# Kernel optimization log

Measured on AMD Instinct MI355X. Metric: run time of the kernel, lower is better.

The kernel has to match this reference:

```python
import jax, jax.numpy as jnp
import numpy as np

N_NODES = 40000


def _gcn_conv(x, edge_index, W, b):
    """PyG GCNConv: add self-loops, symmetric degree normalization,
    linear transform, gather-scale-scatter aggregation, bias."""
    n = x.shape[0]
    loops = jnp.arange(n, dtype=edge_index.dtype)
    src = jnp.concatenate([edge_index[0], loops])  # [E+N]
    dst = jnp.concatenate([edge_index[1], loops])  # [E+N]
    ones = jnp.ones(src.shape[0], dtype=x.dtype)
    deg = jax.ops.segment_sum(ones, dst, num_segments=n)  # in-degree incl. self-loop
    dinv = jnp.where(deg > 0, jax.lax.rsqrt(deg), 0.0)
    norm = dinv[src] * dinv[dst]  # [E+N]
    h = x @ W  # [n, out]
    msg = h[src] * norm[:, None]  # [E+N, out] gather + scale
    out = jax.ops.segment_sum(msg, dst, num_segments=n)  # scatter-add
    return out + b


def setup_inputs() -> dict:
    key = jax.random.key(0)
    k = jax.random.split(key, 6)
    n, din, dh, dout = N_NODES, 128, 128, 64
    x = jax.random.normal(k[0], (n, din), dtype=jnp.float32)
    edge_index = jax.random.randint(k[1], (2, 640000), 0, n, dtype=jnp.int64)
    W1 = jax.random.normal(k[2], (din, dh), dtype=jnp.float32) / np.sqrt(din)
    b1 = jnp.zeros((dh,), dtype=jnp.float32)
    W2 = jax.random.normal(k[3], (dh, dout), dtype=jnp.float32) / np.sqrt(dh)
    b2 = jnp.zeros((dout,), dtype=jnp.float32)
    return {"x": x, "edge_index": edge_index, "W1": W1, "b1": b1, "W2": W2, "b2": b2}


def reference(x, edge_index, W1, b1, W2, b2):
    h = jax.nn.relu(_gcn_conv(x, edge_index, W1, b1))
    return _gcn_conv(h, edge_index, W2, b2)
```

## Files before the change

### kernel.cpp

```cpp
#include <hip/hip_runtime.h>
#include <hip/hip_fp16.h>


#define N_NODES 40000
#define DIN 128
#define DH 128
#define DOUT 64
#define NEDGES 640000
#define CAP 64
#define NBUCKET 2560
#define I4_PER_CHUNK 500
#define NODES_PER_XCD 5000
#define NCVT 1250
#define NWT 8

typedef _Float16 f16x8 __attribute__((ext_vector_type(8)));
typedef float f32x4 __attribute__((ext_vector_type(4)));

__global__ __launch_bounds__(256) void k_bkt_cvt(
    const float* __restrict__ x, _Float16* __restrict__ xh,
    const int4* __restrict__ src4, const int4* __restrict__ dst4,
    int* __restrict__ deg, unsigned short* __restrict__ ssrc,
    const float* __restrict__ W1, const float* __restrict__ W2,
    _Float16* __restrict__ WT1, _Float16* __restrict__ WT2)
{
    if (blockIdx.x < NBUCKET) {
        const int xg = blockIdx.x & 7;
        const int c  = blockIdx.x >> 3;
        const int lo = xg * NODES_PER_XCD, hi = lo + NODES_PER_XCD;
        const int e0 = c * I4_PER_CHUNK, e1 = e0 + I4_PER_CHUNK;
        for (int e = e0 + threadIdx.x; e < e1; e += 256) {
            int4 d = dst4[e];
            int4 s = src4[e];
            if (d.x >= lo && d.x < hi) {
                int p = atomicAdd(&deg[d.x], 1);
                if (p < CAP) ssrc[d.x * CAP + p] = (unsigned short)s.x;
            }
            if (d.y >= lo && d.y < hi) {
                int p = atomicAdd(&deg[d.y], 1);
                if (p < CAP) ssrc[d.y * CAP + p] = (unsigned short)s.y;
            }
            if (d.z >= lo && d.z < hi) {
                int p = atomicAdd(&deg[d.z], 1);
                if (p < CAP) ssrc[d.z * CAP + p] = (unsigned short)s.z;
            }
            if (d.w >= lo && d.w < hi) {
                int p = atomicAdd(&deg[d.w], 1);
                if (p < CAP) ssrc[d.w * CAP + p] = (unsigned short)s.w;
            }
        }
    } else if (blockIdx.x < NBUCKET + NCVT) {
        const size_t base = ((size_t)(blockIdx.x - NBUCKET) * 256 + threadIdx.x) * 16;
        float4 a0 = *(const float4*)(x + base);
        float4 a1 = *(const float4*)(x + base + 4);
        float4 a2 = *(const float4*)(x + base + 8);
        float4 a3 = *(const float4*)(x + base + 12);
        f16x8 o0 = { (_Float16)a0.x, (_Float16)a0.y, (_Float16)a0.z, (_Float16)a0.w,
                     (_Float16)a1.x, (_Float16)a1.y, (_Float16)a1.z, (_Float16)a1.w };
        f16x8 o1 = { (_Float16)a2.x, (_Float16)a2.y, (_Float16)a2.z, (_Float16)a2.w,
                     (_Float16)a3.x, (_Float16)a3.y, (_Float16)a3.z, (_Float16)a3.w };
        *(f16x8*)(xh + base)     = o0;
        *(f16x8*)(xh + base + 8) = o1;
    } else {
        const int b = blockIdx.x - NBUCKET - NCVT;
        for (int i = b * 256 + threadIdx.x; i < DIN * DH; i += NWT * 256) {
            int k = i >> 7, nn = i & 127;
            WT1[nn * DIN + k] = (_Float16)W1[i];
        }
        for (int i = b * 256 + threadIdx.x; i < DH * DOUT; i += NWT * 256) {
            int k = i >> 6, nn = i & 63;
            WT2[nn * DH + k] = (_Float16)W2[i];
        }
    }
}

__global__ __launch_bounds__(256) void k_scale(
    _Float16* __restrict__ xh, const int* __restrict__ deg)
{
    int idx = blockIdx.x * 256 + threadIdx.x;
    int row = idx >> 4;
    float dn = rsqrtf((float)(deg[row] + 1));
    f16x8 v = *(f16x8*)(xh + (size_t)idx * 8);
    f16x8 o;
#pragma unroll
    for (int j = 0; j < 8; ++j) o[j] = (_Float16)((float)v[j] * dn);
    *(f16x8*)(xh + (size_t)idx * 8) = o;
}

__global__ __launch_bounds__(256) void k_agg_g12(
    const int* __restrict__ deg, const unsigned short* __restrict__ ssrc,
    const _Float16* __restrict__ xh, const float* __restrict__ b1,
    const _Float16* __restrict__ WT1, const _Float16* __restrict__ WT2,
    _Float16* __restrict__ h2)
{
    __shared__ _Float16 ys[16][136];
    __shared__ _Float16 zs[16][136];
    const int w = threadIdx.x >> 6;
    const int lane = threadIdx.x & 63;
    const int g  = lane >> 4;
    const int gl = lane & 15;
    const int node0 = blockIdx.x * 16;
    const int node = node0 + w * 4 + g;

    const int dg = deg[node];
    const int cnt = min(dg, CAP);
    const float dn = rsqrtf((float)(dg + 1));

    float ac[8];
    {
        f16x8 self = *(const f16x8*)(xh + (size_t)node * DIN + gl * 8);
#pragma unroll
        for (int j = 0; j < 8; ++j) ac[j] = (float)self[j];
    }
    int mc = cnt;
    mc = max(mc, __shfl_xor(mc, 16));
    mc = max(mc, __shfl_xor(mc, 32));

    const unsigned short* bin = ssrc + (size_t)node * CAP;
    for (int e = 0; e < mc; e += 8) {
        uint4 pk = *(const uint4*)(bin + e);
        int s0 = (int)(pk.x & 0xFFFF), s1 = (int)(pk.x >> 16);
        int s2 = (int)(pk.y & 0xFFFF), s3 = (int)(pk.y >> 16);
        int s4 = (int)(pk.z & 0xFFFF), s5 = (int)(pk.z >> 16);
        int s6 = (int)(pk.w & 0xFFFF), s7 = (int)(pk.w >> 16);
        float m0 = (e + 0 < cnt) ? 1.f : 0.f;  s0 = (e + 0 < cnt) ? s0 : node;
        float m1 = (e + 1 < cnt) ? 1.f : 0.f;  s1 = (e + 1 < cnt) ? s1 : node;
        float m2 = (e + 2 < cnt) ? 1.f : 0.f;  s2 = (e + 2 < cnt) ? s2 : node;
        float m3 = (e + 3 < cnt) ? 1.f : 0.f;  s3 = (e + 3 < cnt) ? s3 : node;
        float m4 = (e + 4 < cnt) ? 1.f : 0.f;  s4 = (e + 4 < cnt) ? s4 : node;
        float m5 = (e + 5 < cnt) ? 1.f : 0.f;  s5 = (e + 5 < cnt) ? s5 : node;
        float m6 = (e + 6 < cnt) ? 1.f : 0.f;  s6 = (e + 6 < cnt) ? s6 : node;
        float m7 = (e + 7 < cnt) ? 1.f : 0.f;  s7 = (e + 7 < cnt) ? s7 : node;
        f16x8 r0 = *(const f16x8*)(xh + (size_t)s0 * DIN + gl * 8);
        f16x8 r1 = *(const f16x8*)(xh + (size_t)s1 * DIN + gl * 8);
        f16x8 r2 = *(const f16x8*)(xh + (size_t)s2 * DIN + gl * 8);
        f16x8 r3 = *(const f16x8*)(xh + (size_t)s3 * DIN + gl * 8);
        f16x8 r4 = *(const f16x8*)(xh + (size_t)s4 * DIN + gl * 8);
        f16x8 r5 = *(const f16x8*)(xh + (size_t)s5 * DIN + gl * 8);
        f16x8 r6 = *(const f16x8*)(xh + (size_t)s6 * DIN + gl * 8);
        f16x8 r7 = *(const f16x8*)(xh + (size_t)s7 * DIN + gl * 8);
#pragma unroll
        for (int j = 0; j < 8; ++j) {
            ac[j] += (m0 * (float)r0[j] + m1 * (float)r1[j])
                   + (m2 * (float)r2[j] + m3 * (float)r3[j]);
            ac[j] += (m4 * (float)r4[j] + m5 * (float)r5[j])
                   + (m6 * (float)r6[j] + m7 * (float)r7[j]);
        }
    }
    {
        f16x8 o;
#pragma unroll
        for (int j = 0; j < 8; ++j) o[j] = (_Float16)(dn * ac[j]);
        *(f16x8*)&ys[w * 4 + g][gl * 8] = o;
    }
    __syncthreads();

    const int m = lane & 15, quad = lane >> 4;
#pragma unroll
    for (int t = 0; t < 2; ++t) {
        const int nt = w * 2 + t;
        f32x4 acc1 = (f32x4){0.f, 0.f, 0.f, 0.f};
#pragma unroll
        for (int ks = 0; ks < 4; ++ks) {
            f16x8 a = *(const f16x8*)&ys[m][ks * 32 + quad * 8];
            f16x8 b = *(const f16x8*)(WT1 + (size_t)(nt * 16 + m) * DIN + ks * 32 + quad * 8);
            acc1 = __builtin_amdgcn_mfma_f32_16x16x32_f16(a, b, acc1, 0, 0, 0);
        }
        float bias = b1[nt * 16 + m];
#pragma unroll
        for (int r = 0; r < 4; ++r) {
            float v = acc1[r] + bias;
            zs[quad * 4 + r][nt * 16 + m] = (_Float16)(v > 0.f ? v : 0.f);
        }
    }
    __syncthreads();

    {
        f32x4 acc2 = (f32x4){0.f, 0.f, 0.f, 0.f};
#pragma unroll
        for (int ks = 0; ks < 4; ++ks) {
            f16x8 a = *(const f16x8*)&zs[m][ks * 32 + quad * 8];
            f16x8 b = *(const f16x8*)(WT2 + (size_t)(w * 16 + m) * DH + ks * 32 + quad * 8);
            acc2 = __builtin_amdgcn_mfma_f32_16x16x32_f16(a, b, acc2, 0, 0, 0);
        }
#pragma unroll
        for (int r = 0; r < 4; ++r) {
            int nrow = node0 + quad * 4 + r;
            float dnr = rsqrtf((float)(deg[nrow] + 1));
            h2[(size_t)nrow * DOUT + w * 16 + m] = (_Float16)(acc2[r] * dnr);
        }
    }
}

__global__ __launch_bounds__(256) void k_agg2(
    const int* __restrict__ deg, const unsigned short* __restrict__ ssrc,
    const _Float16* __restrict__ h2, const float* __restrict__ b2,
    float* __restrict__ out)
{
    const int w = threadIdx.x >> 6;
    const int lane = threadIdx.x & 63;
    const int g  = lane >> 3;
    const int gl = lane & 7;
    const int node = blockIdx.x * 32 + w * 8 + g;

    const int dg = deg[node];
    const int cnt = min(dg, CAP);
    const float dn = rsqrtf((float)(dg + 1));

    float ac[8];
    {
        f16x8 self = *(const f16x8*)(h2 + (size_t)node * DOUT + gl * 8);
#pragma unroll
        for (int j = 0; j < 8; ++j) ac[j] = (float)self[j];
    }
    int mc = cnt;
    mc = max(mc, __shfl_xor(mc, 8));
    mc = max(mc, __shfl_xor(mc, 16));
    mc = max(mc, __shfl_xor(mc, 32));

    const unsigned short* bin = ssrc + (size_t)node * CAP;
    for (int e = 0; e < mc; e += 8) {
        uint4 pk = *(const uint4*)(bin + e);
        int s0 = (int)(pk.x & 0xFFFF), s1 = (int)(pk.x >> 16);
        int s2 = (int)(pk.y & 0xFFFF), s3 = (int)(pk.y >> 16);
        int s4 = (int)(pk.z & 0xFFFF), s5 = (int)(pk.z >> 16);
        int s6 = (int)(pk.w & 0xFFFF), s7 = (int)(pk.w >> 16);
        float m0 = (e + 0 < cnt) ? 1.f : 0.f;  s0 = (e + 0 < cnt) ? s0 : node;
        float m1 = (e + 1 < cnt) ? 1.f : 0.f;  s1 = (e + 1 < cnt) ? s1 : node;
        float m2 = (e + 2 < cnt) ? 1.f : 0.f;  s2 = (e + 2 < cnt) ? s2 : node;
        float m3 = (e + 3 < cnt) ? 1.f : 0.f;  s3 = (e + 3 < cnt) ? s3 : node;
        float m4 = (e + 4 < cnt) ? 1.f : 0.f;  s4 = (e + 4 < cnt) ? s4 : node;
        float m5 = (e + 5 < cnt) ? 1.f : 0.f;  s5 = (e + 5 < cnt) ? s5 : node;
        float m6 = (e + 6 < cnt) ? 1.f : 0.f;  s6 = (e + 6 < cnt) ? s6 : node;
        float m7 = (e + 7 < cnt) ? 1.f : 0.f;  s7 = (e + 7 < cnt) ? s7 : node;
        f16x8 r0 = *(const f16x8*)(h2 + (size_t)s0 * DOUT + gl * 8);
        f16x8 r1 = *(const f16x8*)(h2 + (size_t)s1 * DOUT + gl * 8);
        f16x8 r2 = *(const f16x8*)(h2 + (size_t)s2 * DOUT + gl * 8);
        f16x8 r3 = *(const f16x8*)(h2 + (size_t)s3 * DOUT + gl * 8);
        f16x8 r4 = *(const f16x8*)(h2 + (size_t)s4 * DOUT + gl * 8);
        f16x8 r5 = *(const f16x8*)(h2 + (size_t)s5 * DOUT + gl * 8);
        f16x8 r6 = *(const f16x8*)(h2 + (size_t)s6 * DOUT + gl * 8);
        f16x8 r7 = *(const f16x8*)(h2 + (size_t)s7 * DOUT + gl * 8);
#pragma unroll
        for (int j = 0; j < 8; ++j) {
            ac[j] += (m0 * (float)r0[j] + m1 * (float)r1[j])
                   + (m2 * (float)r2[j] + m3 * (float)r3[j]);
            ac[j] += (m4 * (float)r4[j] + m5 * (float)r5[j])
                   + (m6 * (float)r6[j] + m7 * (float)r7[j]);
        }
    }
    float4 ba = *(const float4*)(b2 + gl * 8);
    float4 bb = *(const float4*)(b2 + gl * 8 + 4);
    float4 o0 = { dn * ac[0] + ba.x, dn * ac[1] + ba.y,
                  dn * ac[2] + ba.z, dn * ac[3] + ba.w };
    float4 o1 = { dn * ac[4] + bb.x, dn * ac[5] + bb.y,
                  dn * ac[6] + bb.z, dn * ac[7] + bb.w };
    float* orow = out + (size_t)node * DOUT + gl * 8;
    *(float4*)orow = o0;
    *(float4*)(orow + 4) = o1;
}

extern "C" void kernel_launch(void* const* d_in, const int* in_sizes, int n_in,
                              void* d_out, int out_size, void* d_ws, size_t ws_size,
                              hipStream_t stream) {
    const float* x  = (const float*)d_in[0];
    const int*   ei = (const int*)d_in[1];
    const float* W1 = (const float*)d_in[2];
    const float* b1 = (const float*)d_in[3];
    const float* W2 = (const float*)d_in[4];
    const float* b2 = (const float*)d_in[5];
    float* out = (float*)d_out;

    const int n = N_NODES, E = NEDGES;
    const int* src = ei;
    const int* dst = ei + E;

    char* ws = (char*)d_ws;
    int*            deg  = (int*)(ws + 0);
    _Float16*       WT1  = (_Float16*)(ws + 163840);
    _Float16*       WT2  = (_Float16*)(ws + 196608);
    unsigned short* ssrc = (unsigned short*)(ws + 212992);
    _Float16*       xh   = (_Float16*)(ws + 5332992);
    _Float16*       h2   = (_Float16*)(ws + 15572992);

    hipMemsetAsync(deg, 0, N_NODES * sizeof(int), stream);
    k_bkt_cvt <<<NBUCKET + NCVT + NWT, 256, 0, stream>>>(x, xh, (const int4*)src,
                                                         (const int4*)dst, deg, ssrc,
                                                         W1, W2, WT1, WT2);
    k_scale   <<<(N_NODES * DIN / 8) / 256, 256, 0, stream>>>(xh, deg);
    k_agg_g12 <<<n / 16, 256, 0, stream>>>(deg, ssrc, xh, b1, WT1, WT2, h2);
    k_agg2    <<<n / 32, 256, 0, stream>>>(deg, ssrc, h2, b2, out);
}
```

Measured before the change: 158.8 us.

## Replicate per-node edge counters and bins four ways to reduce atomic contention

Bucketing now spreads each node's incoming edges over four replica sub-bins of 32 slots, selected by chunk index. Each replica has its own atomic counter, so fewer concurrent atomics hit the same address. Degree becomes the sum of four counters, read as one int4. Both aggregation kernels now loop over the four sub-bins, each padded to a multiple of 8. That adds masked gather iterations and shuffle reductions, enlarges the bin and counter memory and the memset, and caps each replica at 32 edges.

```diff
diff --git a/kernel.cpp b/kernel.cpp
--- a/kernel.cpp
+++ b/kernel.cpp
@@ -7,7 +7,7 @@
 #define DH 128
 #define DOUT 64
 #define NEDGES 640000
-#define CAP 64
+#define CAPR 32
 #define NBUCKET 2560
 #define I4_PER_CHUNK 500
 #define NODES_PER_XCD 5000
@@ -20,33 +20,34 @@
 __global__ __launch_bounds__(256) void k_bkt_cvt(
     const float* __restrict__ x, _Float16* __restrict__ xh,
     const int4* __restrict__ src4, const int4* __restrict__ dst4,
-    int* __restrict__ deg, unsigned short* __restrict__ ssrc,
+    int* __restrict__ dcnt, unsigned short* __restrict__ rbin,
     const float* __restrict__ W1, const float* __restrict__ W2,
     _Float16* __restrict__ WT1, _Float16* __restrict__ WT2)
 {
     if (blockIdx.x < NBUCKET) {
         const int xg = blockIdx.x & 7;
         const int c  = blockIdx.x >> 3;
+        const int rep = c & 3;
         const int lo = xg * NODES_PER_XCD, hi = lo + NODES_PER_XCD;
         const int e0 = c * I4_PER_CHUNK, e1 = e0 + I4_PER_CHUNK;
         for (int e = e0 + threadIdx.x; e < e1; e += 256) {
             int4 d = dst4[e];
             int4 s = src4[e];
             if (d.x >= lo && d.x < hi) {
-                int p = atomicAdd(&deg[d.x], 1);
-                if (p < CAP) ssrc[d.x * CAP + p] = (unsigned short)s.x;
+                int p = atomicAdd(&dcnt[d.x * 4 + rep], 1);
+                if (p < CAPR) rbin[(size_t)d.x * 128 + rep * CAPR + p] = (unsigned short)s.x;
             }
             if (d.y >= lo && d.y < hi) {
-                int p = atomicAdd(&deg[d.y], 1);
-                if (p < CAP) ssrc[d.y * CAP + p] = (unsigned short)s.y;
+                int p = atomicAdd(&dcnt[d.y * 4 + rep], 1);
+                if (p < CAPR) rbin[(size_t)d.y * 128 + rep * CAPR + p] = (unsigned short)s.y;
             }
             if (d.z >= lo && d.z < hi) {
-                int p = atomicAdd(&deg[d.z], 1);
-                if (p < CAP) ssrc[d.z * CAP + p] = (unsigned short)s.z;
+                int p = atomicAdd(&dcnt[d.z * 4 + rep], 1);
+                if (p < CAPR) rbin[(size_t)d.z * 128 + rep * CAPR + p] = (unsigned short)s.z;
             }
             if (d.w >= lo && d.w < hi) {
-                int p = atomicAdd(&deg[d.w], 1);
-                if (p < CAP) ssrc[d.w * CAP + p] = (unsigned short)s.w;
+                int p = atomicAdd(&dcnt[d.w * 4 + rep], 1);
+                if (p < CAPR) rbin[(size_t)d.w * 128 + rep * CAPR + p] = (unsigned short)s.w;
             }
         }
     } else if (blockIdx.x < NBUCKET + NCVT) {
@@ -75,11 +76,12 @@
 }
 
 __global__ __launch_bounds__(256) void k_scale(
-    _Float16* __restrict__ xh, const int* __restrict__ deg)
+    _Float16* __restrict__ xh, const int* __restrict__ dcnt)
 {
     int idx = blockIdx.x * 256 + threadIdx.x;
     int row = idx >> 4;
-    float dn = rsqrtf((float)(deg[row] + 1));
+    int4 dc = *(const int4*)(dcnt + row * 4);
+    float dn = rsqrtf((float)(dc.x + dc.y + dc.z + dc.w + 1));
     f16x8 v = *(f16x8*)(xh + (size_t)idx * 8);
     f16x8 o;
 #pragma unroll
@@ -88,7 +90,7 @@
 }
 
 __global__ __launch_bounds__(256) void k_agg_g12(
-    const int* __restrict__ deg, const unsigned short* __restrict__ ssrc,
+    const int* __restrict__ dcnt, const unsigned short* __restrict__ rbin,
     const _Float16* __restrict__ xh, const float* __restrict__ b1,
     const _Float16* __restrict__ WT1, const _Float16* __restrict__ WT2,
     _Float16* __restrict__ h2)
@@ -102,8 +104,8 @@
     const int node0 = blockIdx.x * 16;
     const int node = node0 + w * 4 + g;
 
-    const int dg = deg[node];
-    const int cnt = min(dg, CAP);
+    const int4 dc = *(const int4*)(dcnt + node * 4);
+    const int dg = dc.x + dc.y + dc.z + dc.w;
     const float dn = rsqrtf((float)(dg + 1));
 
     float ac[8];
@@ -112,39 +114,44 @@
 #pragma unroll
         for (int j = 0; j < 8; ++j) ac[j] = (float)self[j];
     }
-    int mc = cnt;
-    mc = max(mc, __shfl_xor(mc, 16));
-    mc = max(mc, __shfl_xor(mc, 32));
-
-    const unsigned short* bin = ssrc + (size_t)node * CAP;
-    for (int e = 0; e < mc; e += 8) {
-        uint4 pk = *(const uint4*)(bin + e);
-        int s0 = (int)(pk.x & 0xFFFF), s1 = (int)(pk.x >> 16);
-        int s2 = (int)(pk.y & 0xFFFF), s3 = (int)(pk.y >> 16);
-        int s4 = (int)(pk.z & 0xFFFF), s5 = (int)(pk.z >> 16);
-        int s6 = (int)(pk.w & 0xFFFF), s7 = (int)(pk.w >> 16);
-        float m0 = (e + 0 < cnt) ? 1.f : 0.f;  s0 = (e + 0 < cnt) ? s0 : node;
-        float m1 = (e + 1 < cnt) ? 1.f : 0.f;  s1 = (e + 1 < cnt) ? s1 : node;
-        float m2 = (e + 2 < cnt) ? 1.f : 0.f;  s2 = (e + 2 < cnt) ? s2 : node;
-        float m3 = (e + 3 < cnt) ? 1.f : 0.f;  s3 = (e + 3 < cnt) ? s3 : node;
-        float m4 = (e + 4 < cnt) ? 1.f : 0.f;  s4 = (e + 4 < cnt) ? s4 : node;
-        float m5 = (e + 5 < cnt) ? 1.f : 0.f;  s5 = (e + 5 < cnt) ? s5 : node;
-        float m6 = (e + 6 < cnt) ? 1.f : 0.f;  s6 = (e + 6 < cnt) ? s6 : node;
-        float m7 = (e + 7 < cnt) ? 1.f : 0.f;  s7 = (e + 7 < cnt) ? s7 : node;
-        f16x8 r0 = *(const f16x8*)(xh + (size_t)s0 * DIN + gl * 8);
-        f16x8 r1 = *(const f16x8*)(xh + (size_t)s1 * DIN + gl * 8);
-        f16x8 r2 = *(const f16x8*)(xh + (size_t)s2 * DIN + gl * 8);
-        f16x8 r3 = *(const f16x8*)(xh + (size_t)s3 * DIN + gl * 8);
-        f16x8 r4 = *(const f16x8*)(xh + (size_t)s4 * DIN + gl * 8);
-        f16x8 r5 = *(const f16x8*)(xh + (size_t)s5 * DIN + gl * 8);
-        f16x8 r6 = *(const f16x8*)(xh + (size_t)s6 * DIN + gl * 8);
-        f16x8 r7 = *(const f16x8*)(xh + (size_t)s7 * DIN + gl * 8);
-#pragma unroll
-        for (int j = 0; j < 8; ++j) {
-            ac[j] += (m0 * (float)r0[j] + m1 * (float)r1[j])
-                   + (m2 * (float)r2[j] + m3 * (float)r3[j]);
-            ac[j] += (m4 * (float)r4[j] + m5 * (float)r5[j])
-                   + (m6 * (float)r6[j] + m7 * (float)r7[j]);
+    const unsigned short* bin = rbin + (size_t)node * 128;
+#pragma unroll
+    for (int r = 0; r < 4; ++r) {
+        int cr = (r & 1) ? ((r & 2) ? dc.w : dc.y) : ((r & 2) ? dc.z : dc.x);
+        cr = min(cr, CAPR);
+        int mc = cr;
+        mc = max(mc, __shfl_xor(mc, 16));
+        mc = max(mc, __shfl_xor(mc, 32));
+        const unsigned short* sb = bin + r * CAPR;
+        for (int e = 0; e < mc; e += 8) {
+            uint4 pk = *(const uint4*)(sb + e);
+            int s0 = (int)(pk.x & 0xFFFF), s1 = (int)(pk.x >> 16);
+            int s2 = (int)(pk.y & 0xFFFF), s3 = (int)(pk.y >> 16);
+            int s4 = (int)(pk.z & 0xFFFF), s5 = (int)(pk.z >> 16);
+            int s6 = (int)(pk.w & 0xFFFF), s7 = (int)(pk.w >> 16);
+            float m0 = (e + 0 < cr) ? 1.f : 0.f;  s0 = (e + 0 < cr) ? s0 : node;
+            float m1 = (e + 1 < cr) ? 1.f : 0.f;  s1 = (e + 1 < cr) ? s1 : node;
+            float m2 = (e + 2 < cr) ? 1.f : 0.f;  s2 = (e + 2 < cr) ? s2 : node;
+            float m3 = (e + 3 < cr) ? 1.f : 0.f;  s3 = (e + 3 < cr) ? s3 : node;
+            float m4 = (e + 4 < cr) ? 1.f : 0.f;  s4 = (e + 4 < cr) ? s4 : node;
+            float m5 = (e + 5 < cr) ? 1.f : 0.f;  s5 = (e + 5 < cr) ? s5 : node;
+            float m6 = (e + 6 < cr) ? 1.f : 0.f;  s6 = (e + 6 < cr) ? s6 : node;
+            float m7 = (e + 7 < cr) ? 1.f : 0.f;  s7 = (e + 7 < cr) ? s7 : node;
+            f16x8 r0 = *(const f16x8*)(xh + (size_t)s0 * DIN + gl * 8);
+            f16x8 r1 = *(const f16x8*)(xh + (size_t)s1 * DIN + gl * 8);
+            f16x8 r2 = *(const f16x8*)(xh + (size_t)s2 * DIN + gl * 8);
+            f16x8 r3 = *(const f16x8*)(xh + (size_t)s3 * DIN + gl * 8);
+            f16x8 r4 = *(const f16x8*)(xh + (size_t)s4 * DIN + gl * 8);
+            f16x8 r5 = *(const f16x8*)(xh + (size_t)s5 * DIN + gl * 8);
+            f16x8 r6 = *(const f16x8*)(xh + (size_t)s6 * DIN + gl * 8);
+            f16x8 r7 = *(const f16x8*)(xh + (size_t)s7 * DIN + gl * 8);
+#pragma unroll
+            for (int j = 0; j < 8; ++j) {
+                ac[j] += (m0 * (float)r0[j] + m1 * (float)r1[j])
+                       + (m2 * (float)r2[j] + m3 * (float)r3[j]);
+                ac[j] += (m4 * (float)r4[j] + m5 * (float)r5[j])
+                       + (m6 * (float)r6[j] + m7 * (float)r7[j]);
+            }
         }
     }
     {
@@ -186,14 +193,15 @@
 #pragma unroll
         for (int r = 0; r < 4; ++r) {
             int nrow = node0 + quad * 4 + r;
-            float dnr = rsqrtf((float)(deg[nrow] + 1));
+            int4 dc2 = *(const int4*)(dcnt + nrow * 4);
+            float dnr = rsqrtf((float)(dc2.x + dc2.y + dc2.z + dc2.w + 1));
             h2[(size_t)nrow * DOUT + w * 16 + m] = (_Float16)(acc2[r] * dnr);
         }
     }
 }
 
 __global__ __launch_bounds__(256) void k_agg2(
-    const int* __restrict__ deg, const unsigned short* __restrict__ ssrc,
+    const int* __restrict__ dcnt, const unsigned short* __restrict__ rbin,
     const _Float16* __restrict__ h2, const float* __restrict__ b2,
     float* __restrict__ out)
 {
@@ -203,8 +211,8 @@
     const int gl = lane & 7;
     const int node = blockIdx.x * 32 + w * 8 + g;
 
-    const int dg = deg[node];
-    const int cnt = min(dg, CAP);
+    const int4 dc = *(const int4*)(dcnt + node * 4);
+    const int dg = dc.x + dc.y + dc.z + dc.w;
     const float dn = rsqrtf((float)(dg + 1));
 
     float ac[8];
@@ -213,40 +221,45 @@
 #pragma unroll
         for (int j = 0; j < 8; ++j) ac[j] = (float)self[j];
     }
-    int mc = cnt;
-    mc = max(mc, __shfl_xor(mc, 8));
-    mc = max(mc, __shfl_xor(mc, 16));
-    mc = max(mc, __shfl_xor(mc, 32));
-
-    const unsigned short* bin = ssrc + (size_t)node * CAP;
-    for (int e = 0; e < mc; e += 8) {
-        uint4 pk = *(const uint4*)(bin + e);
-        int s0 = (int)(pk.x & 0xFFFF), s1 = (int)(pk.x >> 16);
-        int s2 = (int)(pk.y & 0xFFFF), s3 = (int)(pk.y >> 16);
-        int s4 = (int)(pk.z & 0xFFFF), s5 = (int)(pk.z >> 16);
-        int s6 = (int)(pk.w & 0xFFFF), s7 = (int)(pk.w >> 16);
-        float m0 = (e + 0 < cnt) ? 1.f : 0.f;  s0 = (e + 0 < cnt) ? s0 : node;
-        float m1 = (e + 1 < cnt) ? 1.f : 0.f;  s1 = (e + 1 < cnt) ? s1 : node;
-        float m2 = (e + 2 < cnt) ? 1.f : 0.f;  s2 = (e + 2 < cnt) ? s2 : node;
-        float m3 = (e + 3 < cnt) ? 1.f : 0.f;  s3 = (e + 3 < cnt) ? s3 : node;
-        float m4 = (e + 4 < cnt) ? 1.f : 0.f;  s4 = (e + 4 < cnt) ? s4 : node;
-        float m5 = (e + 5 < cnt) ? 1.f : 0.f;  s5 = (e + 5 < cnt) ? s5 : node;
-        float m6 = (e + 6 < cnt) ? 1.f : 0.f;  s6 = (e + 6 < cnt) ? s6 : node;
-        float m7 = (e + 7 < cnt) ? 1.f : 0.f;  s7 = (e + 7 < cnt) ? s7 : node;
-        f16x8 r0 = *(const f16x8*)(h2 + (size_t)s0 * DOUT + gl * 8);
-        f16x8 r1 = *(const f16x8*)(h2 + (size_t)s1 * DOUT + gl * 8);
-        f16x8 r2 = *(const f16x8*)(h2 + (size_t)s2 * DOUT + gl * 8);
-        f16x8 r3 = *(const f16x8*)(h2 + (size_t)s3 * DOUT + gl * 8);
-        f16x8 r4 = *(const f16x8*)(h2 + (size_t)s4 * DOUT + gl * 8);
-        f16x8 r5 = *(const f16x8*)(h2 + (size_t)s5 * DOUT + gl * 8);
-        f16x8 r6 = *(const f16x8*)(h2 + (size_t)s6 * DOUT + gl * 8);
-        f16x8 r7 = *(const f16x8*)(h2 + (size_t)s7 * DOUT + gl * 8);
-#pragma unroll
-        for (int j = 0; j < 8; ++j) {
-            ac[j] += (m0 * (float)r0[j] + m1 * (float)r1[j])
-                   + (m2 * (float)r2[j] + m3 * (float)r3[j]);
-            ac[j] += (m4 * (float)r4[j] + m5 * (float)r5[j])
-                   + (m6 * (float)r6[j] + m7 * (float)r7[j]);
+    const unsigned short* bin = rbin + (size_t)node * 128;
+#pragma unroll
+    for (int r = 0; r < 4; ++r) {
+        int cr = (r & 1) ? ((r & 2) ? dc.w : dc.y) : ((r & 2) ? dc.z : dc.x);
+        cr = min(cr, CAPR);
+        int mc = cr;
+        mc = max(mc, __shfl_xor(mc, 8));
+        mc = max(mc, __shfl_xor(mc, 16));
+        mc = max(mc, __shfl_xor(mc, 32));
+        const unsigned short* sb = bin + r * CAPR;
+        for (int e = 0; e < mc; e += 8) {
+            uint4 pk = *(const uint4*)(sb + e);
+            int s0 = (int)(pk.x & 0xFFFF), s1 = (int)(pk.x >> 16);
+            int s2 = (int)(pk.y & 0xFFFF), s3 = (int)(pk.y >> 16);
+            int s4 = (int)(pk.z & 0xFFFF), s5 = (int)(pk.z >> 16);
+            int s6 = (int)(pk.w & 0xFFFF), s7 = (int)(pk.w >> 16);
+            float m0 = (e + 0 < cr) ? 1.f : 0.f;  s0 = (e + 0 < cr) ? s0 : node;
+            float m1 = (e + 1 < cr) ? 1.f : 0.f;  s1 = (e + 1 < cr) ? s1 : node;
+            float m2 = (e + 2 < cr) ? 1.f : 0.f;  s2 = (e + 2 < cr) ? s2 : node;
+            float m3 = (e + 3 < cr) ? 1.f : 0.f;  s3 = (e + 3 < cr) ? s3 : node;
+            float m4 = (e + 4 < cr) ? 1.f : 0.f;  s4 = (e + 4 < cr) ? s4 : node;
+            float m5 = (e + 5 < cr) ? 1.f : 0.f;  s5 = (e + 5 < cr) ? s5 : node;
+            float m6 = (e + 6 < cr) ? 1.f : 0.f;  s6 = (e + 6 < cr) ? s6 : node;
+            float m7 = (e + 7 < cr) ? 1.f : 0.f;  s7 = (e + 7 < cr) ? s7 : node;
+            f16x8 r0 = *(const f16x8*)(h2 + (size_t)s0 * DOUT + gl * 8);
+            f16x8 r1 = *(const f16x8*)(h2 + (size_t)s1 * DOUT + gl * 8);
+            f16x8 r2 = *(const f16x8*)(h2 + (size_t)s2 * DOUT + gl * 8);
+            f16x8 r3 = *(const f16x8*)(h2 + (size_t)s3 * DOUT + gl * 8);
+            f16x8 r4 = *(const f16x8*)(h2 + (size_t)s4 * DOUT + gl * 8);
+            f16x8 r5 = *(const f16x8*)(h2 + (size_t)s5 * DOUT + gl * 8);
+            f16x8 r6 = *(const f16x8*)(h2 + (size_t)s6 * DOUT + gl * 8);
+            f16x8 r7 = *(const f16x8*)(h2 + (size_t)s7 * DOUT + gl * 8);
+#pragma unroll
+            for (int j = 0; j < 8; ++j) {
+                ac[j] += (m0 * (float)r0[j] + m1 * (float)r1[j])
+                       + (m2 * (float)r2[j] + m3 * (float)r3[j]);
+                ac[j] += (m4 * (float)r4[j] + m5 * (float)r5[j])
+                       + (m6 * (float)r6[j] + m7 * (float)r7[j]);
+            }
         }
     }
     float4 ba = *(const float4*)(b2 + gl * 8);
@@ -276,18 +289,18 @@
     const int* dst = ei + E;
 
     char* ws = (char*)d_ws;
-    int*            deg  = (int*)(ws + 0);
-    _Float16*       WT1  = (_Float16*)(ws + 163840);
-    _Float16*       WT2  = (_Float16*)(ws + 196608);
-    unsigned short* ssrc = (unsigned short*)(ws + 212992);
-    _Float16*       xh   = (_Float16*)(ws + 5332992);
-    _Float16*       h2   = (_Float16*)(ws + 15572992);
-
-    hipMemsetAsync(deg, 0, N_NODES * sizeof(int), stream);
+    int*            dcnt = (int*)(ws + 0);
+    _Float16*       WT1  = (_Float16*)(ws + 655360);
+    _Float16*       WT2  = (_Float16*)(ws + 688128);
+    unsigned short* rbin = (unsigned short*)(ws + 704512);
+    _Float16*       xh   = (_Float16*)(ws + 11190272);
+    _Float16*       h2   = (_Float16*)(ws + 21676032);
+
+    hipMemsetAsync(dcnt, 0, N_NODES * 4 * sizeof(int), stream);
     k_bkt_cvt <<<NBUCKET + NCVT + NWT, 256, 0, stream>>>(x, xh, (const int4*)src,
-                                                         (const int4*)dst, deg, ssrc,
+                                                         (const int4*)dst, dcnt, rbin,
                                                          W1, W2, WT1, WT2);
-    k_scale   <<<(N_NODES * DIN / 8) / 256, 256, 0, stream>>>(xh, deg);
-    k_agg_g12 <<<n / 16, 256, 0, stream>>>(deg, ssrc, xh, b1, WT1, WT2, h2);
-    k_agg2    <<<n / 32, 256, 0, stream>>>(deg, ssrc, h2, b2, out);
-}
+    k_scale   <<<(N_NODES * DIN / 8) / 256, 256, 0, stream>>>(xh, dcnt);
+    k_agg_g12 <<<n / 16, 256, 0, stream>>>(dcnt, rbin, xh, b1, WT1, WT2, h2);
+    k_agg2    <<<n / 32, 256, 0, stream>>>(dcnt, rbin, h2, b2, out);
+}
```

Result: slower. 166.7 us (+5.0%).

## Move first GEMM before aggregation and fuse it with edge bucketing

Applied to the files above, without the earlier changes.

The layer-1 linear transform (x@W1) now runs in the same kernel as edge bucketing, converting x to fp16 on the fly and writing h1 directly, instead of converting x and doing the GEMM after aggregation. The aggregation kernel then applies bias and ReLU right after gathering, dropping one shared-memory stage and one barrier. The memset and weight transpose are merged into a new init kernel, and bucketing uses fewer, larger chunks. Applying the transform before aggregation changes the fp16 rounding order, and the extra launch adds dependency overhead.

```diff
diff --git a/kernel.cpp b/kernel.cpp
--- a/kernel.cpp
+++ b/kernel.cpp
@@ -8,21 +8,33 @@
 #define DOUT 64
 #define NEDGES 640000
 #define CAP 64
-#define NBUCKET 2560
-#define I4_PER_CHUNK 500
+#define NBUCKET 640
+#define I4_PER_CHUNK 2000
 #define NODES_PER_XCD 5000
-#define NCVT 1250
-#define NWT 8
 
 typedef _Float16 f16x8 __attribute__((ext_vector_type(8)));
 typedef float f32x4 __attribute__((ext_vector_type(4)));
 
-__global__ __launch_bounds__(256) void k_bkt_cvt(
-    const float* __restrict__ x, _Float16* __restrict__ xh,
+__global__ void k_init(int* __restrict__ deg, const float* __restrict__ W1,
+                       const float* __restrict__ W2,
+                       _Float16* __restrict__ WT1, _Float16* __restrict__ WT2, int n) {
+    int i = blockIdx.x * 256 + threadIdx.x;
+    if (i < n) deg[i] = 0;
+    if (i < DIN * DH) {
+        int k = i >> 7, nn = i & 127;
+        WT1[(size_t)nn * DIN + k] = (_Float16)W1[i];
+    }
+    if (i < DH * DOUT) {
+        int k = i >> 6, nn = i & 63;
+        WT2[(size_t)nn * DH + k] = (_Float16)W2[i];
+    }
+}
+
+__global__ __launch_bounds__(256) void k_work1(
+    const float* __restrict__ x, const _Float16* __restrict__ WT,
+    __half* __restrict__ h,
     const int4* __restrict__ src4, const int4* __restrict__ dst4,
-    int* __restrict__ deg, unsigned short* __restrict__ ssrc,
-    const float* __restrict__ W1, const float* __restrict__ W2,
-    _Float16* __restrict__ WT1, _Float16* __restrict__ WT2)
+    int* __restrict__ deg, unsigned short* __restrict__ ssrc)
 {
     if (blockIdx.x < NBUCKET) {
         const int xg = blockIdx.x & 7;
@@ -49,51 +61,56 @@
                 if (p < CAP) ssrc[d.w * CAP + p] = (unsigned short)s.w;
             }
         }
-    } else if (blockIdx.x < NBUCKET + NCVT) {
-        const size_t base = ((size_t)(blockIdx.x - NBUCKET) * 256 + threadIdx.x) * 16;
-        float4 a0 = *(const float4*)(x + base);
-        float4 a1 = *(const float4*)(x + base + 4);
-        float4 a2 = *(const float4*)(x + base + 8);
-        float4 a3 = *(const float4*)(x + base + 12);
-        f16x8 o0 = { (_Float16)a0.x, (_Float16)a0.y, (_Float16)a0.z, (_Float16)a0.w,
-                     (_Float16)a1.x, (_Float16)a1.y, (_Float16)a1.z, (_Float16)a1.w };
-        f16x8 o1 = { (_Float16)a2.x, (_Float16)a2.y, (_Float16)a2.z, (_Float16)a2.w,
-                     (_Float16)a3.x, (_Float16)a3.y, (_Float16)a3.z, (_Float16)a3.w };
-        *(f16x8*)(xh + base)     = o0;
-        *(f16x8*)(xh + base + 8) = o1;
     } else {
-        const int b = blockIdx.x - NBUCKET - NCVT;
-        for (int i = b * 256 + threadIdx.x; i < DIN * DH; i += NWT * 256) {
-            int k = i >> 7, nn = i & 127;
-            WT1[nn * DIN + k] = (_Float16)W1[i];
-        }
-        for (int i = b * 256 + threadIdx.x; i < DH * DOUT; i += NWT * 256) {
-            int k = i >> 6, nn = i & 63;
-            WT2[nn * DH + k] = (_Float16)W2[i];
+        const int wave = (blockIdx.x - NBUCKET) * 4 + (threadIdx.x >> 6);
+        const int lane = threadIdx.x & 63;
+        const int m = lane & 15, quad = lane >> 4;
+
+        f32x4 acc[8];
+#pragma unroll
+        for (int nt = 0; nt < 8; ++nt) acc[nt] = (f32x4){0.f, 0.f, 0.f, 0.f};
+
+        const float* xrow = x + (size_t)(wave * 16 + m) * DIN + quad * 8;
+#pragma unroll
+        for (int ks = 0; ks < 4; ++ks) {
+            float4 xa = *(const float4*)(xrow + ks * 32);
+            float4 xb = *(const float4*)(xrow + ks * 32 + 4);
+            f16x8 a = { (_Float16)xa.x, (_Float16)xa.y, (_Float16)xa.z, (_Float16)xa.w,
+                        (_Float16)xb.x, (_Float16)xb.y, (_Float16)xb.z, (_Float16)xb.w };
+#pragma unroll
+            for (int nt = 0; nt < 8; ++nt) {
+                f16x8 b = *(const f16x8*)(WT + (size_t)(nt * 16 + m) * DIN + ks * 32 + quad * 8);
+                acc[nt] = __builtin_amdgcn_mfma_f32_16x16x32_f16(a, b, acc[nt], 0, 0, 0);
+            }
+        }
+#pragma unroll
+        for (int r = 0; r < 4; ++r) {
+            int orow = wave * 16 + quad * 4 + r;
+#pragma unroll
+            for (int nt = 0; nt < 8; ++nt)
+                h[(size_t)orow * DH + nt * 16 + m] = (__half)acc[nt][r];
         }
     }
 }
 
 __global__ __launch_bounds__(256) void k_scale(
-    _Float16* __restrict__ xh, const int* __restrict__ deg)
+    _Float16* __restrict__ h1, const int* __restrict__ deg)
 {
     int idx = blockIdx.x * 256 + threadIdx.x;
     int row = idx >> 4;
     float dn = rsqrtf((float)(deg[row] + 1));
-    f16x8 v = *(f16x8*)(xh + (size_t)idx * 8);
+    f16x8 v = *(f16x8*)(h1 + (size_t)idx * 8);
     f16x8 o;
 #pragma unroll
     for (int j = 0; j < 8; ++j) o[j] = (_Float16)((float)v[j] * dn);
-    *(f16x8*)(xh + (size_t)idx * 8) = o;
-}
-
-__global__ __launch_bounds__(256) void k_agg_g12(
+    *(f16x8*)(h1 + (size_t)idx * 8) = o;
+}
+
+__global__ __launch_bounds__(256) void k_agg_g2(
     const int* __restrict__ deg, const unsigned short* __restrict__ ssrc,
-    const _Float16* __restrict__ xh, const float* __restrict__ b1,
-    const _Float16* __restrict__ WT1, const _Float16* __restrict__ WT2,
-    _Float16* __restrict__ h2)
-{
-    __shared__ _Float16 ys[16][136];
+    const _Float16* __restrict__ h1, const float* __restrict__ b1,
+    const _Float16* __restrict__ WT2, _Float16* __restrict__ h2)
+{
     __shared__ _Float16 zs[16][136];
     const int w = threadIdx.x >> 6;
     const int lane = threadIdx.x & 63;
@@ -108,7 +125,7 @@
 
     float ac[8];
     {
-        f16x8 self = *(const f16x8*)(xh + (size_t)node * DIN + gl * 8);
+        f16x8 self = *(const f16x8*)(h1 + (size_t)node * DIN + gl * 8);
 #pragma unroll
         for (int j = 0; j < 8; ++j) ac[j] = (float)self[j];
     }
@@ -131,14 +148,14 @@
         float m5 = (e + 5 < cnt) ? 1.f : 0.f;  s5 = (e + 5 < cnt) ? s5 : node;
         float m6 = (e + 6 < cnt) ? 1.f : 0.f;  s6 = (e + 6 < cnt) ? s6 : node;
         float m7 = (e + 7 < cnt) ? 1.f : 0.f;  s7 = (e + 7 < cnt) ? s7 : node;
-        f16x8 r0 = *(const f16x8*)(xh + (size_t)s0 * DIN + gl * 8);
-        f16x8 r1 = *(const f16x8*)(xh + (size_t)s1 * DIN + gl * 8);
-        f16x8 r2 = *(const f16x8*)(xh + (size_t)s2 * DIN + gl * 8);
-        f16x8 r3 = *(const f16x8*)(xh + (size_t)s3 * DIN + gl * 8);
-        f16x8 r4 = *(const f16x8*)(xh + (size_t)s4 * DIN + gl * 8);
-        f16x8 r5 = *(const f16x8*)(xh + (size_t)s5 * DIN + gl * 8);
-        f16x8 r6 = *(const f16x8*)(xh + (size_t)s6 * DIN + gl * 8);
-        f16x8 r7 = *(const f16x8*)(xh + (size_t)s7 * DIN + gl * 8);
+        f16x8 r0 = *(const f16x8*)(h1 + (size_t)s0 * DIN + gl * 8);
+        f16x8 r1 = *(const f16x8*)(h1 + (size_t)s1 * DIN + gl * 8);
+        f16x8 r2 = *(const f16x8*)(h1 + (size_t)s2 * DIN + gl * 8);
+        f16x8 r3 = *(const f16x8*)(h1 + (size_t)s3 * DIN + gl * 8);
+        f16x8 r4 = *(const f16x8*)(h1 + (size_t)s4 * DIN + gl * 8);
+        f16x8 r5 = *(const f16x8*)(h1 + (size_t)s5 * DIN + gl * 8);
+        f16x8 r6 = *(const f16x8*)(h1 + (size_t)s6 * DIN + gl * 8);
+        f16x8 r7 = *(const f16x8*)(h1 + (size_t)s7 * DIN + gl * 8);
 #pragma unroll
         for (int j = 0; j < 8; ++j) {
             ac[j] += (m0 * (float)r0[j] + m1 * (float)r1[j])
@@ -148,34 +165,23 @@
         }
     }
     {
+        float4 ba = *(const float4*)(b1 + gl * 8);
+        float4 bb = *(const float4*)(b1 + gl * 8 + 4);
         f16x8 o;
-#pragma unroll
-        for (int j = 0; j < 8; ++j) o[j] = (_Float16)(dn * ac[j]);
-        *(f16x8*)&ys[w * 4 + g][gl * 8] = o;
+        float v0 = dn * ac[0] + ba.x; o[0] = (_Float16)(v0 > 0.f ? v0 : 0.f);
+        float v1 = dn * ac[1] + ba.y; o[1] = (_Float16)(v1 > 0.f ? v1 : 0.f);
+        float v2 = dn * ac[2] + ba.z; o[2] = (_Float16)(v2 > 0.f ? v2 : 0.f);
+        float v3 = dn * ac[3] + ba.w; o[3] = (_Float16)(v3 > 0.f ? v3 : 0.f);
+        float v4 = dn * ac[4] + bb.x; o[4] = (_Float16)(v4 > 0.f ? v4 : 0.f);
+        float v5 = dn * ac[5] + bb.y; o[5] = (_Float16)(v5 > 0.f ? v5 : 0.f);
+        float v6 = dn * ac[6] + bb.z; o[6] = (_Float16)(v6 > 0.f ? v6 : 0.f);
+        float v7 = dn * ac[7] + bb.w; o[7] = (_Float16)(v7 > 0.f ? v7 : 0.f);
+        *(f16x8*)&zs[w * 4 + g][gl * 8] = o;
     }
     __syncthreads();
 
-    const int m = lane & 15, quad = lane >> 4;
-#pragma unroll
-    for (int t = 0; t < 2; ++t) {
-        const int nt = w * 2 + t;
-        f32x4 acc1 = (f32x4){0.f, 0.f, 0.f, 0.f};
-#pragma unroll
-        for (int ks = 0; ks < 4; ++ks) {
-            f16x8 a = *(const f16x8*)&ys[m][ks * 32 + quad * 8];
-            f16x8 b = *(const f16x8*)(WT1 + (size_t)(nt * 16 + m) * DIN + ks * 32 + quad * 8);
-            acc1 = __builtin_amdgcn_mfma_f32_16x16x32_f16(a, b, acc1, 0, 0, 0);
-        }
-        float bias = b1[nt * 16 + m];
-#pragma unroll
-        for (int r = 0; r < 4; ++r) {
-            float v = acc1[r] + bias;
-            zs[quad * 4 + r][nt * 16 + m] = (_Float16)(v > 0.f ? v : 0.f);
-        }
-    }
-    __syncthreads();
-
-    {
+    {
+        const int m = lane & 15, quad = lane >> 4;
         f32x4 acc2 = (f32x4){0.f, 0.f, 0.f, 0.f};
 #pragma unroll
         for (int ks = 0; ks < 4; ++ks) {
@@ -280,14 +286,14 @@
     _Float16*       WT1  = (_Float16*)(ws + 163840);
     _Float16*       WT2  = (_Float16*)(ws + 196608);
     unsigned short* ssrc = (unsigned short*)(ws + 212992);
-    _Float16*       xh   = (_Float16*)(ws + 5332992);
+    _Float16*       h1   = (_Float16*)(ws + 5332992);
     _Float16*       h2   = (_Float16*)(ws + 15572992);
 
-    hipMemsetAsync(deg, 0, N_NODES * sizeof(int), stream);
-    k_bkt_cvt <<<NBUCKET + NCVT + NWT, 256, 0, stream>>>(x, xh, (const int4*)src,
-                                                         (const int4*)dst, deg, ssrc,
-                                                         W1, W2, WT1, WT2);
-    k_scale   <<<(N_NODES * DIN / 8) / 256, 256, 0, stream>>>(xh, deg);
-    k_agg_g12 <<<n / 16, 256, 0, stream>>>(deg, ssrc, xh, b1, WT1, WT2, h2);
-    k_agg2    <<<n / 32, 256, 0, stream>>>(deg, ssrc, h2, b2, out);
-}
+    k_init   <<<(n + 255) / 256, 256, 0, stream>>>(deg, W1, W2, WT1, WT2, n);
+    k_work1  <<<NBUCKET + 625, 256, 0, stream>>>(x, WT1, (__half*)h1,
+                                                 (const int4*)src, (const int4*)dst,
+                                                 deg, ssrc);
+    k_scale  <<<(N_NODES * DH / 8) / 256, 256, 0, stream>>>(h1, deg);
+    k_agg_g2 <<<n / 16, 256, 0, stream>>>(deg, ssrc, h1, b1, WT2, h2);
+    k_agg2   <<<n / 32, 256, 0, stream>>>(deg, ssrc, h2, b2, out);
+}
```

Result: no change. 157.1 us (median of 2 runs) (-1.1%).
